# Performance work log

Hardware: AMD Instinct MI355X
Metric: run time of the kernel (lower is better)

## Reference

```python
import jax, jax.numpy as jnp
import numpy as np

NEG = jnp.float32(-1e30)  # finite stand-in for -inf in masked max
SLOPE = 0.01              # F.leaky_relu default negative slope


def _lrelu(v):
    return jnp.where(v >= 0, v, SLOPE * v)


def _mlp(pts, w1, b1, w2, b2, w3, b3):
    # pts: [2, N] -> [64, N]; 1x1 Conv1d == pointwise linear over channel dim
    z = _lrelu(w1 @ pts + b1[:, None])
    z = _lrelu(w2 @ z + b2[:, None])
    z = _lrelu(w3 @ z + b3[:, None])
    return z


def setup_inputs() -> dict:
    key = jax.random.key(0)
    ks = jax.random.split(key, 10)
    B, C, H, W = 4, 19, 256, 256
    x = jax.random.randint(ks[0], (B, C, H, W), 0, 2, dtype=jnp.int32)
    # grid exactly as in the torch module: meshgrid of two linspaces, flattened
    g = np.array(np.meshgrid(np.linspace(-1, 1, 256), np.linspace(-1, 1, 256),
                             sparse=False)).astype(np.float32)  # [2,256,256]
    grid = jnp.asarray(g.reshape(2, -1))  # [2, 65536]
    w1 = jax.random.normal(ks[1], (64, 2), jnp.float32) * 0.5
    b1 = jax.random.normal(ks[2], (64,), jnp.float32) * 0.1
    w2 = jax.random.normal(ks[3], (64, 64), jnp.float32) * 0.125
    b2 = jax.random.normal(ks[4], (64,), jnp.float32) * 0.1
    w3 = jax.random.normal(ks[5], (64, 64), jnp.float32) * 0.125
    b3 = jax.random.normal(ks[6], (64,), jnp.float32) * 0.1
    fcw = jax.random.normal(ks[7], (512, 64 * C), jnp.float32)
    fcb = jax.random.normal(ks[8], (512,), jnp.float32) * 0.1
    return {"x": x, "grid": grid, "w1": w1, "b1": b1, "w2": w2, "b2": b2,
            "w3": w3, "b3": b3, "fcw": fcw, "fcb": fcb}


def reference(x, grid, w1, b1, w2, b2, w3, b3, fcw, fcb):
    B, C = x.shape[0], x.shape[1]
    # Pointwise MLP on the shared grid once (grid identical for all b,c)
    feats = _mlp(grid, w1, b1, w2, b2, w3, b3)                 # [64, N]
    # Fallback feature for empty masks: MLP on a single zero point
    zero_feat = _mlp(jnp.zeros((2, 1), feats.dtype),
                     w1, b1, w2, b2, w3, b3)[:, 0]             # [64]
    mask = (x.reshape(B, C, -1) == 1)                          # [B, C, N]
    # Masked max over the ragged point sets, fully vectorized
    masked = jnp.where(mask[:, :, None, :], feats[None, None], NEG)
    z = jnp.max(masked, axis=-1)                               # [B, C, 64]
    empty = ~jnp.any(mask, axis=-1)                            # [B, C]
    z = jnp.where(empty[..., None], zero_feat, z)
    flat = z.reshape(B, C * 64)                                # channel-major cat
    # EqualLinear: weight scaled by 1/sqrt(in_dim) (lr_mul=1)
    scale = jnp.float32(1.0 / np.sqrt(C * 64))
    out = flat @ (fcw * scale).T + fcb                         # [B, 512]
    return jnp.repeat(out[:, None, :], 18, axis=1)             # [B, 18, 512]
```

## Files before the change

kernel.cpp:

```cpp
#include <hip/hip_runtime.h>

#define NPTS  65536
#define NBC   76
#define NREP  8
#define KEYN  4864

__device__ __forceinline__ float lrelu(float v) { return v >= 0.0f ? v : 0.01f * v; }

__device__ __forceinline__ unsigned fkey(float f) {
  unsigned u = __float_as_uint(f);
  return (u & 0x80000000u) ? ~u : (u | 0x80000000u);
}
__device__ __forceinline__ float fdec(unsigned k) {
  return (k & 0x80000000u) ? __uint_as_float(k & 0x7fffffffu) : __uint_as_float(~k);
}

__global__ __launch_bounds__(256) void k1_fused(
    const int* __restrict__ x, const float* __restrict__ grid,
    const float* __restrict__ w1, const float* __restrict__ b1,
    const float* __restrict__ w2, const float* __restrict__ b2,
    const float* __restrict__ w3, const float* __restrict__ b3,
    unsigned* __restrict__ keys)
{
  __shared__ unsigned zt[64 * 68];
  __shared__ unsigned long long mbits[NBC];

  const int t    = threadIdx.x;
  const int lane = t & 63;
  const int wv   = t >> 6;
  const int n0   = blockIdx.x * 64;

  {
    int bc0 = wv * 19;
    #pragma unroll
    for (int i = 0; i < 19; ++i) {
      int bc = bc0 + i;
      int v = x[(bc << 16) + n0 + lane];
      unsigned long long m = __ballot(v == 1);
      if (lane == 0) mbits[bc] = m;
    }
  }

  const int jb = __builtin_amdgcn_readfirstlane(wv * 16);

  {
    float g0 = grid[n0 + lane];
    float g1 = grid[NPTS + n0 + lane];
    #pragma unroll
    for (int jj = 0; jj < 16; ++jj) {
      int j = jb + jj;
      float z = lrelu(w1[2 * j] * g0 + w1[2 * j + 1] * g1 + b1[j]);
      zt[j * 68 + lane] = __float_as_uint(z);
    }
  }
  __syncthreads();

  float acc[16];

  #pragma unroll
  for (int jj = 0; jj < 16; ++jj) acc[jj] = b2[jb + jj];
  #pragma unroll 4
  for (int k = 0; k < 64; ++k) {
    float zv = __uint_as_float(zt[k * 68 + lane]);
    #pragma unroll
    for (int jj = 0; jj < 16; ++jj) acc[jj] += w2[(jb + jj) * 64 + k] * zv;
  }
  __syncthreads();
  #pragma unroll
  for (int jj = 0; jj < 16; ++jj)
    zt[(jb + jj) * 68 + lane] = __float_as_uint(lrelu(acc[jj]));
  __syncthreads();

  #pragma unroll
  for (int jj = 0; jj < 16; ++jj) acc[jj] = b3[jb + jj];
  #pragma unroll 4
  for (int k = 0; k < 64; ++k) {
    float zv = __uint_as_float(zt[k * 68 + lane]);
    #pragma unroll
    for (int jj = 0; jj < 16; ++jj) acc[jj] += w3[(jb + jj) * 64 + k] * zv;
  }
  __syncthreads();
  #pragma unroll
  for (int jj = 0; jj < 16; ++jj)
    zt[(jb + jj) * 68 + lane] = fkey(lrelu(acc[jj]));
  __syncthreads();

  const int kq = t & 15, bg = t >> 4;
  const int bcbase = bg * 5;

  unsigned mlo[5], mhi[5];
  #pragma unroll
  for (int ii = 0; ii < 5; ++ii) {
    int bc = bcbase + ii;
    unsigned long long m = (bc < NBC) ? mbits[bc] : 0ull;
    mlo[ii] = (unsigned)m;
    mhi[ii] = (unsigned)(m >> 32);
  }

  unsigned uacc[5][4];
  #pragma unroll
  for (int ii = 0; ii < 5; ++ii)
    #pragma unroll
    for (int i = 0; i < 4; ++i) uacc[ii][i] = 0u;

  #pragma unroll 2
  for (int np = 0; np < 8; ++np) {
    const int n = np * 4;
    uint4 lo[4], hi[4];
    #pragma unroll
    for (int i = 0; i < 4; ++i) {
      lo[i] = *reinterpret_cast<const uint4*>(&zt[(kq + 16 * i) * 68 + n]);
      hi[i] = *reinterpret_cast<const uint4*>(&zt[(kq + 16 * i) * 68 + n + 32]);
    }
    #pragma unroll
    for (int ii = 0; ii < 5; ++ii) {
      unsigned sl0 = (unsigned)((int)(mlo[ii] << (31 - n)) >> 31);
      unsigned sl1 = (unsigned)((int)(mlo[ii] << (30 - n)) >> 31);
      unsigned sl2 = (unsigned)((int)(mlo[ii] << (29 - n)) >> 31);
      unsigned sl3 = (unsigned)((int)(mlo[ii] << (28 - n)) >> 31);
      unsigned sh0 = (unsigned)((int)(mhi[ii] << (31 - n)) >> 31);
      unsigned sh1 = (unsigned)((int)(mhi[ii] << (30 - n)) >> 31);
      unsigned sh2 = (unsigned)((int)(mhi[ii] << (29 - n)) >> 31);
      unsigned sh3 = (unsigned)((int)(mhi[ii] << (28 - n)) >> 31);
      #pragma unroll
      for (int i = 0; i < 4; ++i) {
        unsigned a = uacc[ii][i];
        a = max(max(a, lo[i].x & sl0), lo[i].y & sl1);
        a = max(max(a, lo[i].z & sl2), lo[i].w & sl3);
        a = max(max(a, hi[i].x & sh0), hi[i].y & sh1);
        a = max(max(a, hi[i].z & sh2), hi[i].w & sh3);
        uacc[ii][i] = a;
      }
    }
  }

  unsigned* krep = keys + (blockIdx.x & (NREP - 1)) * KEYN;
  #pragma unroll
  for (int ii = 0; ii < 5; ++ii) {
    int bc = bcbase + ii;
    if (bc < NBC) {
      #pragma unroll
      for (int i = 0; i < 4; ++i) {
        unsigned v = uacc[ii][i];
        if (v) atomicMax(&krep[bc * 64 + kq + 16 * i], v);
      }
    }
  }
}

__global__ __launch_bounds__(256) void k2_fc(
    const unsigned* __restrict__ keys,
    const float* __restrict__ b1, const float* __restrict__ w2,
    const float* __restrict__ b2, const float* __restrict__ w3,
    const float* __restrict__ b3,
    const float* __restrict__ fcw, const float* __restrict__ fcb,
    float* __restrict__ out)
{
  __shared__ float flat[4864];
  __shared__ float za[64], zb[64], zf[64];
  const int t = threadIdx.x;

  if (t < 64) za[t] = lrelu(b1[t]);
  __syncthreads();
  if (t < 64) {
    float s = b2[t];
    #pragma unroll 8
    for (int k = 0; k < 64; ++k) s += w2[t * 64 + k] * za[k];
    zb[t] = lrelu(s);
  }
  __syncthreads();
  if (t < 64) {
    float s = b3[t];
    #pragma unroll 8
    for (int k = 0; k < 64; ++k) s += w3[t * 64 + k] * zb[k];
    zf[t] = lrelu(s);
  }
  __syncthreads();

  for (int idx = t; idx < 4864; idx += 256) {
    unsigned m = keys[idx];
    #pragma unroll
    for (int r = 1; r < NREP; ++r) m = max(m, keys[r * KEYN + idx]);
    flat[idx] = m ? fdec(m) : zf[idx & 63];
  }
  __syncthreads();

  const int wv = t >> 6, lane = t & 63;
  const int o = blockIdx.x * 4 + wv;
  const float* wrow = fcw + o * 1216;
  float fa0 = 0.f, fa1 = 0.f, fa2 = 0.f, fa3 = 0.f;
  #pragma unroll
  for (int i = 0; i < 19; ++i) {
    int jj = i * 64 + lane;
    float wvv = wrow[jj];
    fa0 += wvv * flat[jj];
    fa1 += wvv * flat[1216 + jj];
    fa2 += wvv * flat[2432 + jj];
    fa3 += wvv * flat[3648 + jj];
  }
  #pragma unroll
  for (int off = 32; off > 0; off >>= 1) {
    fa0 += __shfl_xor(fa0, off);
    fa1 += __shfl_xor(fa1, off);
    fa2 += __shfl_xor(fa2, off);
    fa3 += __shfl_xor(fa3, off);
  }
  const float scale = 0.028676966733820225f;
  float cb = fcb[o];
  if (lane < 18) {
    out[(0 * 18 + lane) * 512 + o] = fa0 * scale + cb;
    out[(1 * 18 + lane) * 512 + o] = fa1 * scale + cb;
    out[(2 * 18 + lane) * 512 + o] = fa2 * scale + cb;
    out[(3 * 18 + lane) * 512 + o] = fa3 * scale + cb;
  }
}

extern "C" void kernel_launch(void* const* d_in, const int* in_sizes, int n_in,
                              void* d_out, int out_size, void* d_ws, size_t ws_size,
                              hipStream_t stream)
{
  const int*   x    = (const int*)d_in[0];
  const float* grid = (const float*)d_in[1];
  const float* w1   = (const float*)d_in[2];
  const float* b1   = (const float*)d_in[3];
  const float* w2   = (const float*)d_in[4];
  const float* b2   = (const float*)d_in[5];
  const float* w3   = (const float*)d_in[6];
  const float* b3   = (const float*)d_in[7];
  const float* fcw  = (const float*)d_in[8];
  const float* fcb  = (const float*)d_in[9];
  float* out = (float*)d_out;

  unsigned* keys = (unsigned*)d_ws;

  hipMemsetAsync(d_ws, 0, NREP * KEYN * sizeof(unsigned), stream);
  hipLaunchKernelGGL(k1_fused, dim3(1024), dim3(256), 0, stream,
                     x, grid, w1, b1, w2, b2, w3, b3, keys);
  hipLaunchKernelGGL(k2_fc, dim3(128), dim3(256), 0, stream,
                     keys, b1, w2, b2, w3, b3, fcw, fcb, out);
}
```

Before: 145.7 us.

## Double block size in fused MLP-maxpool kernel and ping-pong shared buffers

Raises the fused kernel's block from 256 to 512 threads, so each wave computes 8 instead of 16 MLP output channels and each thread reduces 2 instead of 4 feature columns in the masked max. It also adds a second shared buffer so the MLP layers alternate between two buffers, which removes two block barriers. Leaky ReLU becomes a branchless fmax. The aim is more waves in flight and lower per-thread register pressure, at the cost of more shared memory per block and redundant mask and weight loads spread across more waves.

```diff
diff --git a/kernel.cpp b/kernel.cpp
--- a/kernel.cpp
+++ b/kernel.cpp
@@ -5,7 +5,7 @@
 #define NREP  8
 #define KEYN  4864
 
-__device__ __forceinline__ float lrelu(float v) { return v >= 0.0f ? v : 0.01f * v; }
+__device__ __forceinline__ float lrelu(float v) { return fmaxf(v, 0.01f * v); }
 
 __device__ __forceinline__ unsigned fkey(float f) {
   unsigned u = __float_as_uint(f);
@@ -15,14 +15,15 @@
   return (k & 0x80000000u) ? __uint_as_float(k & 0x7fffffffu) : __uint_as_float(~k);
 }
 
-__global__ __launch_bounds__(256) void k1_fused(
+__global__ __launch_bounds__(512, 8) void k1_fused(
     const int* __restrict__ x, const float* __restrict__ grid,
     const float* __restrict__ w1, const float* __restrict__ b1,
     const float* __restrict__ w2, const float* __restrict__ b2,
     const float* __restrict__ w3, const float* __restrict__ b3,
     unsigned* __restrict__ keys)
 {
-  __shared__ unsigned zt[64 * 68];
+  __shared__ unsigned zt1[64 * 68];
+  __shared__ unsigned zt2[64 * 68];
   __shared__ unsigned long long mbits[NBC];
 
   const int t    = threadIdx.x;
@@ -30,62 +31,59 @@
   const int wv   = t >> 6;
   const int n0   = blockIdx.x * 64;
 
-  {
-    int bc0 = wv * 19;
-    #pragma unroll
-    for (int i = 0; i < 19; ++i) {
-      int bc = bc0 + i;
+  #pragma unroll
+  for (int i = 0; i < 10; ++i) {
+    int bc = wv + 8 * i;
+    if (bc < NBC) {
       int v = x[(bc << 16) + n0 + lane];
       unsigned long long m = __ballot(v == 1);
       if (lane == 0) mbits[bc] = m;
     }
   }
 
-  const int jb = __builtin_amdgcn_readfirstlane(wv * 16);
+  const int jb = __builtin_amdgcn_readfirstlane(wv * 8);
 
   {
     float g0 = grid[n0 + lane];
     float g1 = grid[NPTS + n0 + lane];
     #pragma unroll
-    for (int jj = 0; jj < 16; ++jj) {
+    for (int jj = 0; jj < 8; ++jj) {
       int j = jb + jj;
       float z = lrelu(w1[2 * j] * g0 + w1[2 * j + 1] * g1 + b1[j]);
-      zt[j * 68 + lane] = __float_as_uint(z);
-    }
-  }
-  __syncthreads();
-
-  float acc[16];
-
-  #pragma unroll
-  for (int jj = 0; jj < 16; ++jj) acc[jj] = b2[jb + jj];
+      zt1[j * 68 + lane] = __float_as_uint(z);
+    }
+  }
+  __syncthreads();
+
+  float acc[8];
+
+  #pragma unroll
+  for (int jj = 0; jj < 8; ++jj) acc[jj] = b2[jb + jj];
   #pragma unroll 4
   for (int k = 0; k < 64; ++k) {
-    float zv = __uint_as_float(zt[k * 68 + lane]);
-    #pragma unroll
-    for (int jj = 0; jj < 16; ++jj) acc[jj] += w2[(jb + jj) * 64 + k] * zv;
-  }
-  __syncthreads();
-  #pragma unroll
-  for (int jj = 0; jj < 16; ++jj)
-    zt[(jb + jj) * 68 + lane] = __float_as_uint(lrelu(acc[jj]));
-  __syncthreads();
-
-  #pragma unroll
-  for (int jj = 0; jj < 16; ++jj) acc[jj] = b3[jb + jj];
+    float zv = __uint_as_float(zt1[k * 68 + lane]);
+    #pragma unroll
+    for (int jj = 0; jj < 8; ++jj) acc[jj] += w2[(jb + jj) * 64 + k] * zv;
+  }
+  #pragma unroll
+  for (int jj = 0; jj < 8; ++jj)
+    zt2[(jb + jj) * 68 + lane] = __float_as_uint(lrelu(acc[jj]));
+  __syncthreads();
+
+  #pragma unroll
+  for (int jj = 0; jj < 8; ++jj) acc[jj] = b3[jb + jj];
   #pragma unroll 4
   for (int k = 0; k < 64; ++k) {
-    float zv = __uint_as_float(zt[k * 68 + lane]);
-    #pragma unroll
-    for (int jj = 0; jj < 16; ++jj) acc[jj] += w3[(jb + jj) * 64 + k] * zv;
-  }
-  __syncthreads();
-  #pragma unroll
-  for (int jj = 0; jj < 16; ++jj)
-    zt[(jb + jj) * 68 + lane] = fkey(lrelu(acc[jj]));
-  __syncthreads();
-
-  const int kq = t & 15, bg = t >> 4;
+    float zv = __uint_as_float(zt2[k * 68 + lane]);
+    #pragma unroll
+    for (int jj = 0; jj < 8; ++jj) acc[jj] += w3[(jb + jj) * 64 + k] * zv;
+  }
+  #pragma unroll
+  for (int jj = 0; jj < 8; ++jj)
+    zt1[(jb + jj) * 68 + lane] = fkey(lrelu(acc[jj]));
+  __syncthreads();
+
+  const int kq = t & 31, bg = t >> 5;
   const int bcbase = bg * 5;
 
   unsigned mlo[5], mhi[5];
@@ -97,21 +95,17 @@
     mhi[ii] = (unsigned)(m >> 32);
   }
 
-  unsigned uacc[5][4];
-  #pragma unroll
-  for (int ii = 0; ii < 5; ++ii)
-    #pragma unroll
-    for (int i = 0; i < 4; ++i) uacc[ii][i] = 0u;
+  unsigned uacc[5][2];
+  #pragma unroll
+  for (int ii = 0; ii < 5; ++ii) { uacc[ii][0] = 0u; uacc[ii][1] = 0u; }
 
   #pragma unroll 2
   for (int np = 0; np < 8; ++np) {
     const int n = np * 4;
-    uint4 lo[4], hi[4];
-    #pragma unroll
-    for (int i = 0; i < 4; ++i) {
-      lo[i] = *reinterpret_cast<const uint4*>(&zt[(kq + 16 * i) * 68 + n]);
-      hi[i] = *reinterpret_cast<const uint4*>(&zt[(kq + 16 * i) * 68 + n + 32]);
-    }
+    uint4 lo0 = *reinterpret_cast<const uint4*>(&zt1[kq * 68 + n]);
+    uint4 lo1 = *reinterpret_cast<const uint4*>(&zt1[(kq + 32) * 68 + n]);
+    uint4 hi0 = *reinterpret_cast<const uint4*>(&zt1[kq * 68 + n + 32]);
+    uint4 hi1 = *reinterpret_cast<const uint4*>(&zt1[(kq + 32) * 68 + n + 32]);
     #pragma unroll
     for (int ii = 0; ii < 5; ++ii) {
       unsigned sl0 = (unsigned)((int)(mlo[ii] << (31 - n)) >> 31);
@@ -122,15 +116,16 @@
       unsigned sh1 = (unsigned)((int)(mhi[ii] << (30 - n)) >> 31);
       unsigned sh2 = (unsigned)((int)(mhi[ii] << (29 - n)) >> 31);
       unsigned sh3 = (unsigned)((int)(mhi[ii] << (28 - n)) >> 31);
-      #pragma unroll
-      for (int i = 0; i < 4; ++i) {
-        unsigned a = uacc[ii][i];
-        a = max(max(a, lo[i].x & sl0), lo[i].y & sl1);
-        a = max(max(a, lo[i].z & sl2), lo[i].w & sl3);
-        a = max(max(a, hi[i].x & sh0), hi[i].y & sh1);
-        a = max(max(a, hi[i].z & sh2), hi[i].w & sh3);
-        uacc[ii][i] = a;
-      }
+      unsigned a0 = uacc[ii][0], a1 = uacc[ii][1];
+      a0 = max(max(a0, lo0.x & sl0), lo0.y & sl1);
+      a0 = max(max(a0, lo0.z & sl2), lo0.w & sl3);
+      a0 = max(max(a0, hi0.x & sh0), hi0.y & sh1);
+      a0 = max(max(a0, hi0.z & sh2), hi0.w & sh3);
+      a1 = max(max(a1, lo1.x & sl0), lo1.y & sl1);
+      a1 = max(max(a1, lo1.z & sl2), lo1.w & sl3);
+      a1 = max(max(a1, hi1.x & sh0), hi1.y & sh1);
+      a1 = max(max(a1, hi1.z & sh2), hi1.w & sh3);
+      uacc[ii][0] = a0; uacc[ii][1] = a1;
     }
   }
 
@@ -139,11 +134,9 @@
   for (int ii = 0; ii < 5; ++ii) {
     int bc = bcbase + ii;
     if (bc < NBC) {
-      #pragma unroll
-      for (int i = 0; i < 4; ++i) {
-        unsigned v = uacc[ii][i];
-        if (v) atomicMax(&krep[bc * 64 + kq + 16 * i], v);
-      }
+      unsigned v0 = uacc[ii][0], v1 = uacc[ii][1];
+      if (v0) atomicMax(&krep[bc * 64 + kq], v0);
+      if (v1) atomicMax(&krep[bc * 64 + kq + 32], v1);
     }
   }
 }
@@ -234,7 +227,7 @@
   unsigned* keys = (unsigned*)d_ws;
 
   hipMemsetAsync(d_ws, 0, NREP * KEYN * sizeof(unsigned), stream);
-  hipLaunchKernelGGL(k1_fused, dim3(1024), dim3(256), 0, stream,
+  hipLaunchKernelGGL(k1_fused, dim3(1024), dim3(512), 0, stream,
                      x, grid, w1, b1, w2, b2, w3, b3, keys);
   hipLaunchKernelGGL(k2_fc, dim3(128), dim3(256), 0, stream,
                      keys, b1, w2, b2, w3, b3, fcw, fcb, out);
```

Result: faster. 142.2 us (-2.4%).
